# Performance work log

Measured on AMD Instinct MI355X. Metric: run time of the kernel, lower is better.

The kernel has to match this reference:

```python
import jax, jax.numpy as jnp
import numpy as np

BOUND = 1.0
MIN_NEAR = 0.05
NUM_STEPS = 64
UP_STEPS = 64
DENSITY_SCALE = 1.0
N_RAYS = 16384
HIDDEN = 64


def setup_inputs() -> dict:
    key = jax.random.key(0)
    ks = jax.random.split(key, 8)
    # cameras hover near z=2 looking roughly toward -z so rays hit the [-1,1]^3 AABB
    rays_o = jax.random.normal(ks[0], (N_RAYS, 3), jnp.float32) * 0.1 + jnp.array([0.0, 0.0, 2.0])
    rays_d = jax.random.normal(ks[1], (N_RAYS, 3), jnp.float32) * 0.2 + jnp.array([0.0, 0.0, -1.0])
    rays_d = rays_d / jnp.linalg.norm(rays_d, axis=-1, keepdims=True)
    W1 = jax.random.normal(ks[2], (3, HIDDEN), jnp.float32) / jnp.sqrt(3.0)
    b1 = jnp.zeros((HIDDEN,), jnp.float32)
    w_sigma = jax.random.normal(ks[3], (HIDDEN, 1), jnp.float32) / jnp.sqrt(float(HIDDEN))
    b_sigma = jnp.zeros((1,), jnp.float32)
    W_rgb = jax.random.normal(ks[4], (HIDDEN, 3), jnp.float32) / jnp.sqrt(float(HIDDEN))
    b_rgb = jnp.zeros((3,), jnp.float32)
    return {"rays_o": rays_o, "rays_d": rays_d, "W1": W1, "b1": b1,
            "w_sigma": w_sigma, "b_sigma": b_sigma, "W_rgb": W_rgb, "b_rgb": b_rgb}


def near_far_cube(rays_o, rays_d, bound, min_near):
    tmin = (-bound - rays_o) / (rays_d + 1e-15)
    tmax = (bound - rays_o) / (rays_d + 1e-15)
    near = jnp.max(jnp.minimum(tmin, tmax), axis=-1, keepdims=True)
    far = jnp.min(jnp.maximum(tmin, tmax), axis=-1, keepdims=True)
    miss = far < near
    near = jnp.where(miss, 1e9, near)
    far = jnp.where(miss, 1e9, far)
    near = jnp.maximum(near, min_near)
    return near, far


def sample_pdf(bins, weights, n_samples):
    # bins: [N, M+1], weights: [N, M]; deterministic (det=True) inverse-CDF sampling
    weights = weights + 1e-5
    pdf = weights / jnp.sum(weights, -1, keepdims=True)
    cdf = jnp.cumsum(pdf, -1)
    cdf = jnp.concatenate([jnp.zeros_like(cdf[..., :1]), cdf], -1)  # [N, M+1]
    u = jnp.linspace(0.5 / n_samples, 1.0 - 0.5 / n_samples, n_samples, dtype=cdf.dtype)
    u = jnp.broadcast_to(u, cdf.shape[:-1] + (n_samples,))
    inds = jax.vmap(lambda c, uu: jnp.searchsorted(c, uu, side='right'))(cdf, u)
    below = jnp.maximum(inds - 1, 0)
    above = jnp.minimum(inds, cdf.shape[-1] - 1)
    cdf_b = jnp.take_along_axis(cdf, below, -1)
    cdf_a = jnp.take_along_axis(cdf, above, -1)
    bins_b = jnp.take_along_axis(bins, below, -1)
    bins_a = jnp.take_along_axis(bins, above, -1)
    denom = cdf_a - cdf_b
    denom = jnp.where(denom < 1e-5, jnp.ones_like(denom), denom)
    t = (u - cdf_b) / denom
    return bins_b + t * (bins_a - bins_b)


def mlp(pts, W1, b1, w_sigma, b_sigma, W_rgb, b_rgb):
    h = jax.nn.relu(pts @ W1 + b1)                      # [N, T, HIDDEN]
    sigma = jax.nn.softplus(h @ w_sigma + b_sigma)[..., 0]  # [N, T]
    rgb = jax.nn.sigmoid(h @ W_rgb + b_rgb)             # [N, T, 3]
    return sigma, rgb


def alpha_composite_weights(z_vals, sigma, sample_dist):
    deltas = z_vals[..., 1:] - z_vals[..., :-1]
    deltas = jnp.concatenate([deltas, jnp.broadcast_to(sample_dist, deltas[..., :1].shape)], -1)
    alphas = 1.0 - jnp.exp(-deltas * DENSITY_SCALE * sigma)
    trans = jnp.cumprod(jnp.concatenate([jnp.ones_like(alphas[..., :1]), 1.0 - alphas + 1e-15], -1)[..., :-1], -1)
    return alphas * trans


def reference(rays_o, rays_d, W1, b1, w_sigma, b_sigma, W_rgb, b_rgb):
    rays_d = rays_d / jnp.linalg.norm(rays_d, axis=-1, keepdims=True)
    near, far = near_far_cube(rays_o, rays_d, BOUND, MIN_NEAR)  # [N,1]
    sample_dist = (far - near) / NUM_STEPS                      # [N,1]

    # coarse stratified (deterministic) samples
    z = jnp.linspace(0.0, 1.0, NUM_STEPS, dtype=rays_o.dtype)
    z_vals = near + (far - near) * z                            # [N,T]
    xyzs = rays_o[:, None, :] + rays_d[:, None, :] * z_vals[..., None]
    xyzs = jnp.clip(xyzs, -BOUND, BOUND)
    sigma, _ = mlp(xyzs, W1, b1, w_sigma, b_sigma, W_rgb, b_rgb)
    weights = alpha_composite_weights(z_vals, sigma, sample_dist)

    # inverse-CDF importance resampling (no-grad in original)
    z_mid = 0.5 * (z_vals[..., :-1] + z_vals[..., 1:])          # [N,T-1]
    new_z = sample_pdf(z_mid, weights[:, 1:-1], UP_STEPS)       # [N,UP]
    new_z = jax.lax.stop_gradient(new_z)

    z_all = jnp.sort(jnp.concatenate([z_vals, new_z], -1), -1)  # [N,T+UP]
    xyzs_all = rays_o[:, None, :] + rays_d[:, None, :] * z_all[..., None]
    xyzs_all = jnp.clip(xyzs_all, -BOUND, BOUND)
    sigma_all, rgb_all = mlp(xyzs_all, W1, b1, w_sigma, b_sigma, W_rgb, b_rgb)
    weights_all = alpha_composite_weights(z_all, sigma_all, sample_dist)

    weights_sum = jnp.sum(weights_all, -1)                      # [N]
    image = jnp.sum(weights_all[..., None] * rgb_all, axis=-2)  # [N,3]
    image = image + (1.0 - weights_sum)[..., None]              # white background
    return image
```

## Files before the change

kernel.cpp:

```cpp
#include <hip/hip_runtime.h>
#include <math.h>

#define WAVES_PER_BLOCK 4

typedef float v2f __attribute__((ext_vector_type(2)));
typedef float v4f __attribute__((ext_vector_type(4)));

__device__ __forceinline__ v2f v2_fma(v2f a, v2f b, v2f c) {
    return __builtin_elementwise_fma(a, b, c);
}
__device__ __forceinline__ v2f v2_max0(v2f a) {
    return __builtin_elementwise_max(a, (v2f){0.0f, 0.0f});
}
__device__ __forceinline__ v2f v2_splat(float x) { return (v2f){x, x}; }

__device__ __forceinline__ float fast_rcp(float x) { return __builtin_amdgcn_rcpf(x); }

#define DPP_ROW_SHR(n)  (0x110 | (n))
#define DPP_WF_SL1      0x130
#define DPP_WF_SR1      0x138
#define DPP_ROW_BCAST15 0x142
#define DPP_ROW_BCAST31 0x143

template <int CTRL, int RM = 0xf, int BM = 0xf, bool BC = false>
__device__ __forceinline__ float fdpp(float old_, float src) {
    return __int_as_float(__builtin_amdgcn_update_dpp(
        __float_as_int(old_), __float_as_int(src), CTRL, RM, BM, BC));
}

__device__ __forceinline__ float lane63_bcast(float x) {
    return __int_as_float(__builtin_amdgcn_readlane(__float_as_int(x), 63));
}

__device__ __forceinline__ float scan_add_dpp(float x) {
    x += fdpp<DPP_ROW_SHR(1)>(0.0f, x);
    x += fdpp<DPP_ROW_SHR(2)>(0.0f, x);
    x += fdpp<DPP_ROW_SHR(4)>(0.0f, x);
    x += fdpp<DPP_ROW_SHR(8)>(0.0f, x);
    x += fdpp<DPP_ROW_BCAST15, 0xa>(0.0f, x);
    x += fdpp<DPP_ROW_BCAST31, 0xc>(0.0f, x);
    return x;
}
__device__ __forceinline__ float scan_mul_dpp(float x) {
    x *= fdpp<DPP_ROW_SHR(1)>(1.0f, x);
    x *= fdpp<DPP_ROW_SHR(2)>(1.0f, x);
    x *= fdpp<DPP_ROW_SHR(4)>(1.0f, x);
    x *= fdpp<DPP_ROW_SHR(8)>(1.0f, x);
    x *= fdpp<DPP_ROW_BCAST15, 0xa>(1.0f, x);
    x *= fdpp<DPP_ROW_BCAST31, 0xc>(1.0f, x);
    return x;
}
__device__ __forceinline__ float wave_sum_dpp(float x) {
    return lane63_bcast(scan_add_dpp(x));
}

__device__ __forceinline__ float softplus_f(float x) {
    return fmaxf(x, 0.0f) + __logf(1.0f + __expf(-fabsf(x)));
}
__device__ __forceinline__ float sigmoid_f(float x) {
    return fast_rcp(1.0f + __expf(-x));
}
__device__ __forceinline__ float clamp1(float x) {
    return fminf(fmaxf(x, -1.0f), 1.0f);
}

__device__ __forceinline__ int count_lt64(const float* a, float x) {
    int lo = 0, hi = 64;
    while (lo < hi) { int mid = (lo + hi) >> 1; if (a[mid] < x) lo = mid + 1; else hi = mid; }
    return lo;
}
__device__ __forceinline__ int count_le64(const float* a, float x) {
    int lo = 0, hi = 64;
    while (lo < hi) { int mid = (lo + hi) >> 1; if (a[mid] <= x) lo = mid + 1; else hi = mid; }
    return lo;
}

__global__ __launch_bounds__(WAVES_PER_BLOCK * 64)
void nerf_render_kernel(const float* __restrict__ rays_o,
                        const float* __restrict__ rays_d,
                        const float* __restrict__ W1,
                        const float* __restrict__ b1,
                        const float* __restrict__ w_sigma,
                        const float* __restrict__ b_sigma,
                        const float* __restrict__ W_rgb,
                        const float* __restrict__ b_rgb,
                        float* __restrict__ out)
{
    const int tid  = threadIdx.x;
    const int lane = tid & 63;
    const int wv   = tid >> 6;
    const int ray  = blockIdx.x * WAVES_PER_BLOCK + wv;

    __shared__ float s_cm  [WAVES_PER_BLOCK][128];
    __shared__ float s_zmid[WAVES_PER_BLOCK][64];
    __shared__ float s_cdf [WAVES_PER_BLOCK][64];
    __shared__ float s_zall[WAVES_PER_BLOCK][128];

    float ox = rays_o[ray * 3 + 0], oy = rays_o[ray * 3 + 1], oz = rays_o[ray * 3 + 2];
    float dx = rays_d[ray * 3 + 0], dy = rays_d[ray * 3 + 1], dz = rays_d[ray * 3 + 2];
    {
        float inv = __builtin_amdgcn_rsqf(dx * dx + dy * dy + dz * dz);
        dx *= inv; dy *= inv; dz *= inv;
    }

    float rx = fast_rcp(dx + 1e-15f);
    float ry = fast_rcp(dy + 1e-15f);
    float rz = fast_rcp(dz + 1e-15f);
    float t0x = (-1.0f - ox) * rx, t1x = (1.0f - ox) * rx;
    float t0y = (-1.0f - oy) * ry, t1y = (1.0f - oy) * ry;
    float t0z = (-1.0f - oz) * rz, t1z = (1.0f - oz) * rz;
    float nearv = fmaxf(fmaxf(fminf(t0x, t1x), fminf(t0y, t1y)), fminf(t0z, t1z));
    float farv  = fminf(fminf(fmaxf(t0x, t1x), fmaxf(t0y, t1y)), fmaxf(t0z, t1z));
    const bool miss = (farv < nearv);
    if (miss) { nearv = 1e9f; farv = 1e9f; }
    nearv = fmaxf(nearv, 0.05f);
    const float sample_dist = (farv - nearv) * (1.0f / 64.0f);

    const float bs0 = b_sigma[0];
    const float br0 = b_rgb[0], br1 = b_rgb[1], br2 = b_rgb[2];

    {
        float w1x = W1[lane], w1y = W1[64 + lane], w1z = W1[128 + lane];
        float eox = ox, eoy = oy, eoz = oz, msc = 1.0f;
        if (miss) {
            eox = clamp1(fmaf(dx, 1e9f, ox));
            eoy = clamp1(fmaf(dy, 1e9f, oy));
            eoz = clamp1(fmaf(dz, 1e9f, oz));
            msc = 0.0f;
        }
        float cj = fmaf(eox, w1x, fmaf(eoy, w1y, fmaf(eoz, w1z, b1[lane])));
        float mj = msc * fmaf(dx, w1x, fmaf(dy, w1y, dz * w1z));
        int g = (lane >> 1) * 4 + (lane & 1);
        s_cm[wv][g]     = cj;
        s_cm[wv][g + 2] = mj;
    }

    float z = nearv + (farv - nearv) * ((float)lane * (1.0f / 63.0f));

    const v2f* ws2 = (const v2f*)w_sigma;
    v2f z2 = v2_splat(z);
    v2f acc = (v2f){bs0, 0.0f};
#pragma unroll 8
    for (int t = 0; t < 32; ++t) {
        v4f g = *(const v4f*)&s_cm[wv][4 * t];
        v2f h = v2_max0(v2_fma((v2f){g.z, g.w}, z2, (v2f){g.x, g.y}));
        acc = v2_fma(h, ws2[t], acc);
    }
    float sigma = softplus_f(acc.x + acc.y);

    float z_next = fdpp<DPP_WF_SL1>(0.0f, z);
    float delta  = (lane < 63) ? (z_next - z) : sample_dist;
    float alpha  = 1.0f - __expf(-delta * sigma);
    float v      = 1.0f - alpha + 1e-15f;
    float incl   = scan_mul_dpp(v);
    float trans  = fdpp<DPP_WF_SR1>(1.0f, incl);
    float w = alpha * trans;

    float wgt = (lane >= 1 && lane <= 62) ? (w + 1e-5f) : 0.0f;
    float cumw = scan_add_dpp(wgt);
    float total = lane63_bcast(cumw);
    float cdf_incl = cumw * fast_rcp(total);

    float zmid = 0.5f * (z + z_next);
    s_zmid[wv][lane] = (lane < 63) ? zmid : 0.0f;
    s_cdf [wv][lane] = (lane < 63) ? cdf_incl : 2.0f;
    __syncthreads();

    float u = 0.0078125f + (float)lane * 0.015625f;
    int ind = count_le64(s_cdf[wv], u);
    int below = ind - 1;
    int above = (ind < 62) ? ind : 62;
    float cb = s_cdf[wv][below], ca = s_cdf[wv][above];
    float bb = s_zmid[wv][below], ba = s_zmid[wv][above];
    float denom = ca - cb;
    if (denom < 1e-5f) denom = 1.0f;
    float t = (u - cb) * fast_rcp(denom);
    float nz = fmaf(t, ba - bb, bb);

    __syncthreads();

    s_zmid[wv][lane] = z;
    s_cdf [wv][lane] = nz;
    __syncthreads();
    int pa = lane + count_lt64(s_cdf [wv], z);
    int pb = lane + count_le64(s_zmid[wv], nz);
    s_zall[wv][pa] = z;
    s_zall[wv][pb] = nz;
    __syncthreads();

    float za0 = s_zall[wv][2 * lane + 0];
    float za1 = s_zall[wv][2 * lane + 1];

    v2f zz = (v2f){za0, za1};
    v2f s2 = v2_splat(bs0);
    v2f r2 = v2_splat(br0), g2 = v2_splat(br1), bch2 = v2_splat(br2);
#pragma unroll 8
    for (int t = 0; t < 32; ++t) {
        v4f g = *(const v4f*)&s_cm[wv][4 * t];
        int j0 = 2 * t, j1 = 2 * t + 1;
        v2f h0 = v2_max0(v2_fma(v2_splat(g.z), zz, v2_splat(g.x)));
        s2   = v2_fma(h0, v2_splat(w_sigma[j0]),       s2);
        r2   = v2_fma(h0, v2_splat(W_rgb[3 * j0 + 0]), r2);
        g2   = v2_fma(h0, v2_splat(W_rgb[3 * j0 + 1]), g2);
        bch2 = v2_fma(h0, v2_splat(W_rgb[3 * j0 + 2]), bch2);
        v2f h1 = v2_max0(v2_fma(v2_splat(g.w), zz, v2_splat(g.y)));
        s2   = v2_fma(h1, v2_splat(w_sigma[j1]),       s2);
        r2   = v2_fma(h1, v2_splat(W_rgb[3 * j1 + 0]), r2);
        g2   = v2_fma(h1, v2_splat(W_rgb[3 * j1 + 1]), g2);
        bch2 = v2_fma(h1, v2_splat(W_rgb[3 * j1 + 2]), bch2);
    }
    float sg0 = softplus_f(s2.x), sg1 = softplus_f(s2.y);
    float r0 = sigmoid_f(r2.x),   r1 = sigmoid_f(r2.y);
    float g0 = sigmoid_f(g2.x),   g1 = sigmoid_f(g2.y);
    float bl0 = sigmoid_f(bch2.x), bl1 = sigmoid_f(bch2.y);

    float zn0 = fdpp<DPP_WF_SL1>(0.0f, za0);
    float d0 = za1 - za0;
    float d1 = (lane < 63) ? (zn0 - za1) : sample_dist;
    float a0 = 1.0f - __expf(-d0 * sg0);
    float a1 = 1.0f - __expf(-d1 * sg1);
    float v0 = 1.0f - a0 + 1e-15f;
    float v1 = 1.0f - a1 + 1e-15f;
    float local = v0 * v1;
    float incl2 = scan_mul_dpp(local);
    float eprod = fdpp<DPP_WF_SR1>(1.0f, incl2);
    float w0 = a0 * eprod;
    float w1 = a1 * (eprod * v0);

    float wsum = wave_sum_dpp(w0 + w1);
    float rs   = wave_sum_dpp(fmaf(w0, r0,  w1 * r1));
    float gs   = wave_sum_dpp(fmaf(w0, g0,  w1 * g1));
    float bs   = wave_sum_dpp(fmaf(w0, bl0, w1 * bl1));

    if (lane == 0) {
        float bg = 1.0f - wsum;
        out[ray * 3 + 0] = rs + bg;
        out[ray * 3 + 1] = gs + bg;
        out[ray * 3 + 2] = bs + bg;
    }
}

extern "C" void kernel_launch(void* const* d_in, const int* in_sizes, int n_in,
                              void* d_out, int out_size, void* d_ws, size_t ws_size,
                              hipStream_t stream) {
    const float* rays_o  = (const float*)d_in[0];
    const float* rays_d  = (const float*)d_in[1];
    const float* W1      = (const float*)d_in[2];
    const float* b1      = (const float*)d_in[3];
    const float* w_sigma = (const float*)d_in[4];
    const float* b_sigma = (const float*)d_in[5];
    const float* W_rgb   = (const float*)d_in[6];
    const float* b_rgb   = (const float*)d_in[7];
    float* out = (float*)d_out;

    const int n_rays = in_sizes[0] / 3;
    dim3 grid((n_rays + WAVES_PER_BLOCK - 1) / WAVES_PER_BLOCK);
    dim3 block(WAVES_PER_BLOCK * 64);
    hipLaunchKernelGGL(nerf_render_kernel, grid, block, 0, stream,
                       rays_o, rays_d, W1, b1, w_sigma, b_sigma, W_rgb, b_rgb, out);
}
```

Before: 96.06 us.

## Use fp16 MFMA for second-pass MLP output layer and drop block barriers

Replaces the scalar FMA loop for the 128-sample second MLP pass with 16x16x32 fp16 MFMA instructions. Hidden activations are packed to fp16 per lane and the output weights are preloaded as B fragments, with results staged through a new shared buffer. Block-wide __syncthreads are removed since each wave uses only its own shared-memory slice, and launch bounds now request higher occupancy. This trades fp32 precision for fp16 in the hidden/output product, and relies on implicit wave-level ordering of LDS accesses without explicit barriers.

After: 99.23 us. +3.3%, slower.

```diff
diff --git a/kernel.cpp b/kernel.cpp
--- a/kernel.cpp
+++ b/kernel.cpp
@@ -5,6 +5,8 @@
 
 typedef float v2f __attribute__((ext_vector_type(2)));
 typedef float v4f __attribute__((ext_vector_type(4)));
+typedef __fp16 fp16v2 __attribute__((ext_vector_type(2)));
+typedef _Float16 half8 __attribute__((ext_vector_type(8)));
 
 __device__ __forceinline__ v2f v2_fma(v2f a, v2f b, v2f c) {
     return __builtin_elementwise_fma(a, b, c);
@@ -75,7 +77,7 @@
     return lo;
 }
 
-__global__ __launch_bounds__(WAVES_PER_BLOCK * 64)
+__global__ __launch_bounds__(WAVES_PER_BLOCK * 64, 8)
 void nerf_render_kernel(const float* __restrict__ rays_o,
                         const float* __restrict__ rays_d,
                         const float* __restrict__ W1,
@@ -90,11 +92,27 @@
     const int lane = tid & 63;
     const int wv   = tid >> 6;
     const int ray  = blockIdx.x * WAVES_PER_BLOCK + wv;
+    const int r15  = lane & 15;
+    const int kgrp = lane >> 4;
 
     __shared__ float s_cm  [WAVES_PER_BLOCK][128];
     __shared__ float s_zmid[WAVES_PER_BLOCK][64];
     __shared__ float s_cdf [WAVES_PER_BLOCK][64];
     __shared__ float s_zall[WAVES_PER_BLOCK][128];
+    __shared__ float s_out [WAVES_PER_BLOCK][4 * 132];
+
+    half8 bfrag[2];
+#pragma unroll
+    for (int q = 0; q < 2; ++q) {
+#pragma unroll
+        for (int j = 0; j < 8; ++j) {
+            int k = q * 32 + kgrp * 8 + j;
+            float wval = 0.0f;
+            if (r15 == 0)      wval = w_sigma[k];
+            else if (r15 < 4)  wval = W_rgb[3 * k + (r15 - 1)];
+            bfrag[q][j] = (_Float16)wval;
+        }
+    }
 
     float ox = rays_o[ray * 3 + 0], oy = rays_o[ray * 3 + 1], oz = rays_o[ray * 3 + 2];
     float dx = rays_d[ray * 3 + 0], dy = rays_d[ray * 3 + 1], dz = rays_d[ray * 3 + 2];
@@ -138,15 +156,15 @@
     float z = nearv + (farv - nearv) * ((float)lane * (1.0f / 63.0f));
 
     const v2f* ws2 = (const v2f*)w_sigma;
-    v2f z2 = v2_splat(z);
-    v2f acc = (v2f){bs0, 0.0f};
+    v2f z2c = v2_splat(z);
+    v2f acc0 = (v2f){bs0, 0.0f};
 #pragma unroll 8
     for (int t = 0; t < 32; ++t) {
         v4f g = *(const v4f*)&s_cm[wv][4 * t];
-        v2f h = v2_max0(v2_fma((v2f){g.z, g.w}, z2, (v2f){g.x, g.y}));
-        acc = v2_fma(h, ws2[t], acc);
-    }
-    float sigma = softplus_f(acc.x + acc.y);
+        v2f h = v2_max0(v2_fma((v2f){g.z, g.w}, z2c, (v2f){g.x, g.y}));
+        acc0 = v2_fma(h, ws2[t], acc0);
+    }
+    float sigma = softplus_f(acc0.x + acc0.y);
 
     float z_next = fdpp<DPP_WF_SL1>(0.0f, z);
     float delta  = (lane < 63) ? (z_next - z) : sample_dist;
@@ -164,7 +182,6 @@
     float zmid = 0.5f * (z + z_next);
     s_zmid[wv][lane] = (lane < 63) ? zmid : 0.0f;
     s_cdf [wv][lane] = (lane < 63) ? cdf_incl : 2.0f;
-    __syncthreads();
 
     float u = 0.0078125f + (float)lane * 0.015625f;
     int ind = count_le64(s_cdf[wv], u);
@@ -177,42 +194,54 @@
     float t = (u - cb) * fast_rcp(denom);
     float nz = fmaf(t, ba - bb, bb);
 
-    __syncthreads();
-
     s_zmid[wv][lane] = z;
     s_cdf [wv][lane] = nz;
-    __syncthreads();
     int pa = lane + count_lt64(s_cdf [wv], z);
     int pb = lane + count_le64(s_zmid[wv], nz);
     s_zall[wv][pa] = z;
     s_zall[wv][pb] = nz;
-    __syncthreads();
 
     float za0 = s_zall[wv][2 * lane + 0];
     float za1 = s_zall[wv][2 * lane + 1];
 
-    v2f zz = (v2f){za0, za1};
-    v2f s2 = v2_splat(bs0);
-    v2f r2 = v2_splat(br0), g2 = v2_splat(br1), bch2 = v2_splat(br2);
-#pragma unroll 8
-    for (int t = 0; t < 32; ++t) {
-        v4f g = *(const v4f*)&s_cm[wv][4 * t];
-        int j0 = 2 * t, j1 = 2 * t + 1;
-        v2f h0 = v2_max0(v2_fma(v2_splat(g.z), zz, v2_splat(g.x)));
-        s2   = v2_fma(h0, v2_splat(w_sigma[j0]),       s2);
-        r2   = v2_fma(h0, v2_splat(W_rgb[3 * j0 + 0]), r2);
-        g2   = v2_fma(h0, v2_splat(W_rgb[3 * j0 + 1]), g2);
-        bch2 = v2_fma(h0, v2_splat(W_rgb[3 * j0 + 2]), bch2);
-        v2f h1 = v2_max0(v2_fma(v2_splat(g.w), zz, v2_splat(g.y)));
-        s2   = v2_fma(h1, v2_splat(w_sigma[j1]),       s2);
-        r2   = v2_fma(h1, v2_splat(W_rgb[3 * j1 + 0]), r2);
-        g2   = v2_fma(h1, v2_splat(W_rgb[3 * j1 + 1]), g2);
-        bch2 = v2_fma(h1, v2_splat(W_rgb[3 * j1 + 2]), bch2);
-    }
-    float sg0 = softplus_f(s2.x), sg1 = softplus_f(s2.y);
-    float r0 = sigmoid_f(r2.x),   r1 = sigmoid_f(r2.y);
-    float g0 = sigmoid_f(g2.x),   g1 = sigmoid_f(g2.y);
-    float bl0 = sigmoid_f(bch2.x), bl1 = sigmoid_f(bch2.y);
+    {
+        float biasv = (r15 == 0) ? bs0 : (r15 == 1) ? br0 : (r15 == 2) ? br1
+                     : (r15 == 3) ? br2 : 0.0f;
+        v4f accInit = (v4f){biasv, biasv, biasv, biasv};
+#pragma unroll 2
+        for (int mt = 0; mt < 8; ++mt) {
+            const int Mbase = mt * 16;
+            float zs = s_zall[wv][Mbase + r15];
+            v2f zz = v2_splat(zs);
+            v4f acc = accInit;
+#pragma unroll
+            for (int q = 0; q < 2; ++q) {
+                half8 afrag;
+#pragma unroll
+                for (int g4 = 0; g4 < 4; ++g4) {
+                    v4f g = *(const v4f*)&s_cm[wv][4 * (q * 16 + kgrp * 4 + g4)];
+                    v2f hp = v2_max0(v2_fma((v2f){g.z, g.w}, zz, (v2f){g.x, g.y}));
+                    fp16v2 pk = __builtin_amdgcn_cvt_pkrtz(hp.x, hp.y);
+                    afrag[2 * g4]     = (_Float16)pk.x;
+                    afrag[2 * g4 + 1] = (_Float16)pk.y;
+                }
+                acc = __builtin_amdgcn_mfma_f32_16x16x32_f16(afrag, bfrag[q], acc, 0, 0, 0);
+            }
+            if (r15 < 4) {
+                *(v4f*)&s_out[wv][r15 * 132 + Mbase + kgrp * 4] = acc;
+            }
+        }
+    }
+
+    v2f sgp = *(const v2f*)&s_out[wv][0 * 132 + 2 * lane];
+    v2f rp  = *(const v2f*)&s_out[wv][1 * 132 + 2 * lane];
+    v2f gp  = *(const v2f*)&s_out[wv][2 * 132 + 2 * lane];
+    v2f bp  = *(const v2f*)&s_out[wv][3 * 132 + 2 * lane];
+
+    float sg0 = softplus_f(sgp.x), sg1 = softplus_f(sgp.y);
+    float r0 = sigmoid_f(rp.x),   r1 = sigmoid_f(rp.y);
+    float g0 = sigmoid_f(gp.x),   g1 = sigmoid_f(gp.y);
+    float bl0 = sigmoid_f(bp.x),  bl1 = sigmoid_f(bp.y);
 
     float zn0 = fdpp<DPP_WF_SL1>(0.0f, za0);
     float d0 = za1 - za0;
```
